# Performance work log

Measured on AMD Instinct MI355X. Metric: run time of the kernel, lower is better.

Reference implementation:

```python
import jax, jax.numpy as jnp
import numpy as np


def setup_inputs() -> dict:
    key = jax.random.key(0)
    k1, k2, k3 = jax.random.split(key, 3)
    B, T, D = 8, 2048, 128      # *A = (B, T), address_size = D
    N, V = 4096, 512            # num_addresses, *B = (V,)
    return {
        "selector": jax.random.normal(k1, (B, T, D), dtype=jnp.float32),
        "param_bank": jax.random.normal(k2, (N, V), dtype=jnp.float32),
        "address_space": jax.random.normal(k3, (N, D), dtype=jnp.float32),
    }


def reference(selector, param_bank, address_space):
    # scores: [B, T, N] = selector @ address_space^T (unscaled)
    scores = jnp.einsum("btd,nd->btn", selector, address_space)
    weights = jax.nn.softmax(scores, axis=-1)
    # weighted sum over the bank: [B, T, V]
    return jnp.einsum("btn,nv->btv", weights, param_bank)
```

## Files before the change

kernel.cpp:

```cpp
#include <hip/hip_runtime.h>

typedef __attribute__((ext_vector_type(8))) short bf16x8;
typedef __attribute__((ext_vector_type(8))) _Float16 f16x8;
typedef __attribute__((ext_vector_type(2))) __fp16 fp16v2;
typedef __attribute__((ext_vector_type(16))) float f32x16;

#define DDIM 128
#define NADDR 4096
#define VDIM 512
#define MTOT 16384
#define NT 32
#define NTILES (NADDR/NT)
#define NSPLIT 8
#define LOG2E 1.44269504088896340736f

__device__ __forceinline__ unsigned pkhi(float hi, float lo){
  return __builtin_amdgcn_perm(__float_as_uint(hi), __float_as_uint(lo), 0x07060302u);
}

__global__ __launch_bounds__(512)
void prep_k(const float* __restrict__ addr, _Float16* __restrict__ kt)
{
  const int nt = blockIdx.x, ts = threadIdx.x;
  const int r = ts >> 4, c8 = (ts & 15) * 8;
  const float* s = addr + (size_t)(nt*NT + r)*DDIM + c8;
  float4 a = *(const float4*)s;
  float4 b = *(const float4*)(s + 4);
  union { f16x8 v; fp16v2 h[4]; } u;
  u.h[0] = __builtin_amdgcn_cvt_pkrtz(a.x, a.y);
  u.h[1] = __builtin_amdgcn_cvt_pkrtz(a.z, a.w);
  u.h[2] = __builtin_amdgcn_cvt_pkrtz(b.x, b.y);
  u.h[3] = __builtin_amdgcn_cvt_pkrtz(b.z, b.w);
  ((f16x8*)kt)[(size_t)nt*512 + ts] = u.v;
}

__global__ __launch_bounds__(1024)
void prep_v(const float* __restrict__ bank, short* __restrict__ vt)
{
  const int nt = blockIdx.x, t = threadIdx.x;
  const int vv = t & 511, half = t >> 9;
  const float* src = bank + (size_t)(nt*NT + half*16) * VDIM + vv;
  float v[16];
  #pragma unroll
  for (int k = 0; k < 16; ++k) v[k] = src[(size_t)k * VDIM];
  uint4 p0, p1;
  p0.x = pkhi(v[1],  v[0]);  p0.y = pkhi(v[3],  v[2]);
  p0.z = pkhi(v[5],  v[4]);  p0.w = pkhi(v[7],  v[6]);
  p1.x = pkhi(v[9],  v[8]);  p1.y = pkhi(v[11], v[10]);
  p1.z = pkhi(v[13], v[12]); p1.w = pkhi(v[15], v[14]);
  uint4* dst = (uint4*)vt + ((size_t)nt*1024 + t)*2;
  dst[0] = p0; dst[1] = p1;
}

__global__ __launch_bounds__(256, 4)
void pass1_kernel(const float* __restrict__ sel,
                  const _Float16* __restrict__ kt,
                  short* __restrict__ pt,
                  float* __restrict__ den,
                  int m_off)
{
  __shared__ __align__(16) _Float16 sK[2][32][136];

  const int tid  = threadIdx.x;
  const int wave = tid >> 6;
  const int lane = tid & 63;
  const int h    = lane >> 5;
  const int c32  = lane & 31;

  const int nq  = blockIdx.x & 7;
  const int mbl = blockIdx.x >> 3;
  const int m0  = m_off + mbl * 128;
  const int wm  = wave * 32;
  const int mtl = mbl * 4 + wave;

  f16x8 aQ[8];
  {
    const float* q = sel + (size_t)(m0 + wm + c32) * DDIM + 8*h;
    #pragma unroll
    for (int ks = 0; ks < 8; ++ks){
      float4 a = *(const float4*)(q + 16*ks);
      float4 b = *(const float4*)(q + 16*ks + 4);
      f16x8 f;
      f[0]=(_Float16)(a.x*LOG2E); f[1]=(_Float16)(a.y*LOG2E);
      f[2]=(_Float16)(a.z*LOG2E); f[3]=(_Float16)(a.w*LOG2E);
      f[4]=(_Float16)(b.x*LOG2E); f[5]=(_Float16)(b.y*LOG2E);
      f[6]=(_Float16)(b.z*LOG2E); f[7]=(_Float16)(b.w*LOG2E);
      aQ[ks] = f;
    }
  }

  f32x16 zc;
  #pragma unroll
  for (int r=0;r<16;++r) zc[r] = 0.f;
  asm volatile("" : "+v"(zc));

  float lacc = 0.f;

  const int kr = tid >> 4, kc = (tid & 15) * 8;
  const f16x8* kbase = (const f16x8*)kt + (size_t)(nq*16)*512;
  bf16x8* pbase = (bf16x8*)pt + (size_t)mtl * NTILES * 128;

  f16x8 kfr[2];
  kfr[0] = kbase[tid];
  kfr[1] = kbase[tid + 256];

  for (int t = 0; t < 16; ++t){
    const int b = t & 1;

    *(f16x8*)&sK[b][kr]     [kc] = kfr[0];
    *(f16x8*)&sK[b][kr + 16][kc] = kfr[1];
    __syncthreads();

    {
      const int t1 = (t+1) & 15;
      kfr[0] = kbase[(size_t)t1*512 + tid];
      kfr[1] = kbase[(size_t)t1*512 + tid + 256];
    }

    __builtin_amdgcn_s_setprio(1);
    f32x16 sAcc0, sAcc1;
    {
      f16x8 aK0 = *(const f16x8*)&sK[b][c32][8*h];
      f16x8 aK1 = *(const f16x8*)&sK[b][c32][16 + 8*h];
      sAcc0 = __builtin_amdgcn_mfma_f32_32x32x16_f16(aK0, aQ[0], zc, 0,0,0);
      sAcc1 = __builtin_amdgcn_mfma_f32_32x32x16_f16(aK1, aQ[1], zc, 0,0,0);
    }
    #pragma unroll
    for (int ks=1; ks<4; ++ks){
      f16x8 aK0 = *(const f16x8*)&sK[b][c32][16*(2*ks)   + 8*h];
      f16x8 aK1 = *(const f16x8*)&sK[b][c32][16*(2*ks+1) + 8*h];
      sAcc0 = __builtin_amdgcn_mfma_f32_32x32x16_f16(aK0, aQ[2*ks],   sAcc0, 0,0,0);
      sAcc1 = __builtin_amdgcn_mfma_f32_32x32x16_f16(aK1, aQ[2*ks+1], sAcc1, 0,0,0);
    }
    __builtin_amdgcn_s_setprio(0);

    unsigned dw[2][4];
    #pragma unroll
    for (int j=0;j<2;++j)
      #pragma unroll
      for (int i=0;i<4;++i){
        float pa = __builtin_amdgcn_exp2f(sAcc0[8*j + 2*i]     + sAcc1[8*j + 2*i]);
        float pb = __builtin_amdgcn_exp2f(sAcc0[8*j + 2*i + 1] + sAcc1[8*j + 2*i + 1]);
        lacc += __uint_as_float(__float_as_uint(pa) & 0xffff0000u);
        lacc += __uint_as_float(__float_as_uint(pb) & 0xffff0000u);
        dw[j][i] = pkhi(pb, pa);
      }

    const int nt = nq*16 + t;
    #pragma unroll
    for (int j=0;j<2;++j){
      auto s02 = __builtin_amdgcn_permlane32_swap(dw[j][0], dw[j][2], false, false);
      auto s13 = __builtin_amdgcn_permlane32_swap(dw[j][1], dw[j][3], false, false);
      union { unsigned u[4]; bf16x8 v; } ap;
      ap.u[0] = s02[0]; ap.u[1] = s13[0]; ap.u[2] = s02[1]; ap.u[3] = s13[1];
      pbase[((size_t)nt*64 + lane)*2 + j] = ap.v;
    }
  }

  float tot = lacc + __shfl_xor(lacc, 32);
  if (lane < 32)
    den[(size_t)(m0 + wm + c32)*8 + nq] = tot;
}

#define P2_LOAD(NTI, A0, A1, B)                                          \
  { const size_t nto = (size_t)(NTI);                                    \
    A0 = pa[(nto*64 + lane)*2];                                          \
    A1 = pa[(nto*64 + lane)*2 + 1];                                      \
    _Pragma("unroll")                                                    \
    for (int j=0;j<2;++j)                                                \
      _Pragma("unroll")                                                  \
      for (int jv=0;jv<4;++jv)                                           \
        B[j*4+jv] = vb[nto*2048 + (size_t)((j*512) + v0 + 32*jv + c32)*2 + h]; }

#define P2_MM(A0, A1, B)                                                 \
  { _Pragma("unroll")                                                    \
    for (int jv=0;jv<4;++jv)                                             \
      oAcc[jv] = __builtin_amdgcn_mfma_f32_32x32x16_bf16(A0, B[jv],      \
                                                         oAcc[jv], 0,0,0); \
    _Pragma("unroll")                                                    \
    for (int jv=0;jv<4;++jv)                                             \
      oAcc[jv] = __builtin_amdgcn_mfma_f32_32x32x16_bf16(A1, B[4+jv],    \
                                                         oAcc[jv], 0,0,0); }

__global__ __launch_bounds__(256, 2)
void pass2_kernel(const short* __restrict__ pt,
                  const short* __restrict__ vt,
                  const float* __restrict__ den,
                  float* __restrict__ out,
                  int m_off)
{
  const int tid  = threadIdx.x;
  const int wave = tid >> 6;
  const int lane = tid & 63;
  const int h    = lane >> 5;
  const int c32  = lane & 31;

  const int vblk = blockIdx.x & 3;
  const int mb   = blockIdx.x >> 2;
  const int v0   = vblk * 128;
  const int mtl  = mb * 4 + wave;
  const int mg   = m_off + mtl * 32;

  const bf16x8* pa = (const bf16x8*)pt + (size_t)mtl * NTILES * 128;
  const bf16x8* vb = (const bf16x8*)vt;

  f32x16 oAcc[4];
  #pragma unroll
  for (int jv=0;jv<4;++jv)
    #pragma unroll
    for (int r=0;r<16;++r) oAcc[jv][r] = 0.f;

  bf16x8 A0a, A1a, Ba[8];
  bf16x8 A0b, A1b, Bb[8];

  P2_LOAD(0, A0a, A1a, Ba);
  for (int nt = 0; nt < NTILES; nt += 2){
    P2_LOAD(nt+1, A0b, A1b, Bb);
    P2_MM(A0a, A1a, Ba);
    if (nt + 2 < NTILES) P2_LOAD(nt+2, A0a, A1a, Ba);
    P2_MM(A0b, A1b, Bb);
  }

  #pragma unroll
  for (int r=0;r<16;++r){
    const int mrow = (r&3) + 8*(r>>2) + 4*h;
    const int m = mg + mrow;
    float4 d0 = *(const float4*)&den[(size_t)m*8];
    float4 d1 = *(const float4*)&den[(size_t)m*8 + 4];
    const float inv = 1.0f / (d0.x+d0.y+d0.z+d0.w + d1.x+d1.y+d1.z+d1.w);
    float* op = out + (size_t)m * VDIM + v0 + c32;
    #pragma unroll
    for (int jv=0;jv<4;++jv)
      op[32*jv] = oAcc[jv][r] * inv;
  }
}

extern "C" void kernel_launch(void* const* d_in, const int* in_sizes, int n_in,
                              void* d_out, int out_size, void* d_ws, size_t ws_size,
                              hipStream_t stream) {
  const float* sel  = (const float*)d_in[0];
  const float* bank = (const float*)d_in[1];
  const float* addr = (const float*)d_in[2];
  float* out = (float*)d_out;

  char* ws = (char*)d_ws;
  _Float16* kt  = (_Float16*)ws;
  short*    vt  = (short*)(ws + (1u<<20));
  float*    den = (float*)(ws + (5u<<20));
  short*    pt  = (short*)(ws + (6u<<20));

  int CM = MTOT;
  while (CM > 2048 && (size_t)(6u<<20) + (size_t)CM*NADDR*2 > ws_size) CM >>= 1;

  hipLaunchKernelGGL(prep_k, dim3(NTILES), dim3(512),  0, stream, addr, kt);
  hipLaunchKernelGGL(prep_v, dim3(NTILES), dim3(1024), 0, stream, bank, vt);
  for (int mo = 0; mo < MTOT; mo += CM){
    hipLaunchKernelGGL(pass1_kernel, dim3(CM/16), dim3(256), 0, stream,
                       sel, kt, pt, den, mo);
    hipLaunchKernelGGL(pass2_kernel, dim3(CM/32), dim3(256), 0, stream,
                       pt, vt, den, out, mo);
  }
}
```

Before: 227.3 us.

## Load K fragments directly from global and regroup pass2 waves by row tile

prep_k now writes K in MFMA-fragment order, so pass1 loads operands straight from global memory into registers. This removes the LDS double buffer and the per-tile __syncthreads. pass2 is reorganised so each 512-thread block covers one 32-row tile, with eight waves each owning 64 V columns. The P tile is then shared across waves through cache, each wave holds fewer accumulators, and register pressure drops. The cost is more global or L2 traffic for K and V fragments, and no LDS reuse in pass1.

```diff
diff --git a/kernel.cpp b/kernel.cpp
--- a/kernel.cpp
+++ b/kernel.cpp
@@ -11,7 +11,6 @@
 #define MTOT 16384
 #define NT 32
 #define NTILES (NADDR/NT)
-#define NSPLIT 8
 #define LOG2E 1.44269504088896340736f
 
 __device__ __forceinline__ unsigned pkhi(float hi, float lo){
@@ -22,8 +21,8 @@
 void prep_k(const float* __restrict__ addr, _Float16* __restrict__ kt)
 {
   const int nt = blockIdx.x, ts = threadIdx.x;
-  const int r = ts >> 4, c8 = (ts & 15) * 8;
-  const float* s = addr + (size_t)(nt*NT + r)*DDIM + c8;
+  const int ks = ts >> 6, r = (ts >> 1) & 31, hh = ts & 1;
+  const float* s = addr + (size_t)(nt*NT + r)*DDIM + 16*ks + 8*hh;
   float4 a = *(const float4*)s;
   float4 b = *(const float4*)(s + 4);
   union { f16x8 v; fp16v2 h[4]; } u;
@@ -59,8 +58,6 @@
                   float* __restrict__ den,
                   int m_off)
 {
-  __shared__ __align__(16) _Float16 sK[2][32][136];
-
   const int tid  = threadIdx.x;
   const int wave = tid >> 6;
   const int lane = tid & 63;
@@ -96,41 +93,24 @@
 
   float lacc = 0.f;
 
-  const int kr = tid >> 4, kc = (tid & 15) * 8;
-  const f16x8* kbase = (const f16x8*)kt + (size_t)(nq*16)*512;
+  const f16x8* kb = (const f16x8*)kt + (size_t)(nq*16)*512;
   bf16x8* pbase = (bf16x8*)pt + (size_t)mtl * NTILES * 128;
-
-  f16x8 kfr[2];
-  kfr[0] = kbase[tid];
-  kfr[1] = kbase[tid + 256];
+  const int fl = c32*2 + h;
 
   for (int t = 0; t < 16; ++t){
-    const int b = t & 1;
-
-    *(f16x8*)&sK[b][kr]     [kc] = kfr[0];
-    *(f16x8*)&sK[b][kr + 16][kc] = kfr[1];
-    __syncthreads();
-
-    {
-      const int t1 = (t+1) & 15;
-      kfr[0] = kbase[(size_t)t1*512 + tid];
-      kfr[1] = kbase[(size_t)t1*512 + tid + 256];
-    }
+    f16x8 aK[8];
+    #pragma unroll
+    for (int ks=0;ks<8;++ks)
+      aK[ks] = kb[(size_t)t*512 + ks*64 + fl];
 
     __builtin_amdgcn_s_setprio(1);
     f32x16 sAcc0, sAcc1;
-    {
-      f16x8 aK0 = *(const f16x8*)&sK[b][c32][8*h];
-      f16x8 aK1 = *(const f16x8*)&sK[b][c32][16 + 8*h];
-      sAcc0 = __builtin_amdgcn_mfma_f32_32x32x16_f16(aK0, aQ[0], zc, 0,0,0);
-      sAcc1 = __builtin_amdgcn_mfma_f32_32x32x16_f16(aK1, aQ[1], zc, 0,0,0);
-    }
+    sAcc0 = __builtin_amdgcn_mfma_f32_32x32x16_f16(aK[0], aQ[0], zc, 0,0,0);
+    sAcc1 = __builtin_amdgcn_mfma_f32_32x32x16_f16(aK[1], aQ[1], zc, 0,0,0);
     #pragma unroll
     for (int ks=1; ks<4; ++ks){
-      f16x8 aK0 = *(const f16x8*)&sK[b][c32][16*(2*ks)   + 8*h];
-      f16x8 aK1 = *(const f16x8*)&sK[b][c32][16*(2*ks+1) + 8*h];
-      sAcc0 = __builtin_amdgcn_mfma_f32_32x32x16_f16(aK0, aQ[2*ks],   sAcc0, 0,0,0);
-      sAcc1 = __builtin_amdgcn_mfma_f32_32x32x16_f16(aK1, aQ[2*ks+1], sAcc1, 0,0,0);
+      sAcc0 = __builtin_amdgcn_mfma_f32_32x32x16_f16(aK[2*ks],   aQ[2*ks],   sAcc0, 0,0,0);
+      sAcc1 = __builtin_amdgcn_mfma_f32_32x32x16_f16(aK[2*ks+1], aQ[2*ks+1], sAcc1, 0,0,0);
     }
     __builtin_amdgcn_s_setprio(0);
 
@@ -162,27 +142,7 @@
     den[(size_t)(m0 + wm + c32)*8 + nq] = tot;
 }
 
-#define P2_LOAD(NTI, A0, A1, B)                                          \
-  { const size_t nto = (size_t)(NTI);                                    \
-    A0 = pa[(nto*64 + lane)*2];                                          \
-    A1 = pa[(nto*64 + lane)*2 + 1];                                      \
-    _Pragma("unroll")                                                    \
-    for (int j=0;j<2;++j)                                                \
-      _Pragma("unroll")                                                  \
-      for (int jv=0;jv<4;++jv)                                           \
-        B[j*4+jv] = vb[nto*2048 + (size_t)((j*512) + v0 + 32*jv + c32)*2 + h]; }
-
-#define P2_MM(A0, A1, B)                                                 \
-  { _Pragma("unroll")                                                    \
-    for (int jv=0;jv<4;++jv)                                             \
-      oAcc[jv] = __builtin_amdgcn_mfma_f32_32x32x16_bf16(A0, B[jv],      \
-                                                         oAcc[jv], 0,0,0); \
-    _Pragma("unroll")                                                    \
-    for (int jv=0;jv<4;++jv)                                             \
-      oAcc[jv] = __builtin_amdgcn_mfma_f32_32x32x16_bf16(A1, B[4+jv],    \
-                                                         oAcc[jv], 0,0,0); }
-
-__global__ __launch_bounds__(256, 2)
+__global__ __launch_bounds__(512, 2)
 void pass2_kernel(const short* __restrict__ pt,
                   const short* __restrict__ vt,
                   const float* __restrict__ den,
@@ -195,31 +155,46 @@
   const int h    = lane >> 5;
   const int c32  = lane & 31;
 
-  const int vblk = blockIdx.x & 3;
-  const int mb   = blockIdx.x >> 2;
-  const int v0   = vblk * 128;
-  const int mtl  = mb * 4 + wave;
-  const int mg   = m_off + mtl * 32;
+  const int mtl = blockIdx.x;
+  const int v0  = wave * 64;
+  const int mg  = m_off + mtl * 32;
 
   const bf16x8* pa = (const bf16x8*)pt + (size_t)mtl * NTILES * 128;
   const bf16x8* vb = (const bf16x8*)vt;
 
-  f32x16 oAcc[4];
-  #pragma unroll
-  for (int jv=0;jv<4;++jv)
+  f32x16 oAcc[2];
+  #pragma unroll
+  for (int jv=0;jv<2;++jv)
     #pragma unroll
     for (int r=0;r<16;++r) oAcc[jv][r] = 0.f;
 
-  bf16x8 A0a, A1a, Ba[8];
-  bf16x8 A0b, A1b, Bb[8];
-
-  P2_LOAD(0, A0a, A1a, Ba);
+  bf16x8 A0a, A1a, B00a, B01a, B10a, B11a;
+  bf16x8 A0b, A1b, B00b, B01b, B10b, B11b;
+
+#define P2L(NTI, A0, A1, B00, B01, B10, B11)                              \
+  { const size_t o = (size_t)(NTI);                                       \
+    A0  = pa[(o*64 + lane)*2];                                            \
+    A1  = pa[(o*64 + lane)*2 + 1];                                        \
+    B00 = vb[o*2048 + (size_t)(      v0      + c32)*2 + h];               \
+    B01 = vb[o*2048 + (size_t)(      v0 + 32 + c32)*2 + h];               \
+    B10 = vb[o*2048 + (size_t)(512 + v0      + c32)*2 + h];               \
+    B11 = vb[o*2048 + (size_t)(512 + v0 + 32 + c32)*2 + h]; }
+
+#define P2M(A0, A1, B00, B01, B10, B11)                                   \
+  { oAcc[0] = __builtin_amdgcn_mfma_f32_32x32x16_bf16(A0, B00, oAcc[0], 0,0,0); \
+    oAcc[1] = __builtin_amdgcn_mfma_f32_32x32x16_bf16(A0, B01, oAcc[1], 0,0,0); \
+    oAcc[0] = __builtin_amdgcn_mfma_f32_32x32x16_bf16(A1, B10, oAcc[0], 0,0,0); \
+    oAcc[1] = __builtin_amdgcn_mfma_f32_32x32x16_bf16(A1, B11, oAcc[1], 0,0,0); }
+
+  P2L(0, A0a, A1a, B00a, B01a, B10a, B11a);
   for (int nt = 0; nt < NTILES; nt += 2){
-    P2_LOAD(nt+1, A0b, A1b, Bb);
-    P2_MM(A0a, A1a, Ba);
-    if (nt + 2 < NTILES) P2_LOAD(nt+2, A0a, A1a, Ba);
-    P2_MM(A0b, A1b, Bb);
-  }
+    P2L(nt+1, A0b, A1b, B00b, B01b, B10b, B11b);
+    P2M(A0a, A1a, B00a, B01a, B10a, B11a);
+    if (nt + 2 < NTILES) P2L(nt+2, A0a, A1a, B00a, B01a, B10a, B11a);
+    P2M(A0b, A1b, B00b, B01b, B10b, B11b);
+  }
+#undef P2L
+#undef P2M
 
   #pragma unroll
   for (int r=0;r<16;++r){
@@ -229,9 +204,8 @@
     float4 d1 = *(const float4*)&den[(size_t)m*8 + 4];
     const float inv = 1.0f / (d0.x+d0.y+d0.z+d0.w + d1.x+d1.y+d1.z+d1.w);
     float* op = out + (size_t)m * VDIM + v0 + c32;
-    #pragma unroll
-    for (int jv=0;jv<4;++jv)
-      op[32*jv] = oAcc[jv][r] * inv;
+    op[0]  = oAcc[0][r] * inv;
+    op[32] = oAcc[1][r] * inv;
   }
 }
 
@@ -257,7 +231,7 @@
   for (int mo = 0; mo < MTOT; mo += CM){
     hipLaunchKernelGGL(pass1_kernel, dim3(CM/16), dim3(256), 0, stream,
                        sel, kt, pt, den, mo);
-    hipLaunchKernelGGL(pass2_kernel, dim3(CM/32), dim3(256), 0, stream,
+    hipLaunchKernelGGL(pass2_kernel, dim3(CM/32), dim3(512), 0, stream,
                        pt, vt, den, out, mo);
   }
 }
```

Result: slower. 234.5 us (+3.2%).
